# Optimization experiments

Measured on AMD Instinct MI355X. Metric: run time of the kernel, lower is better.

The kernel has to match this reference:

```python
import jax, jax.numpy as jnp
import numpy as np

N = 100000
HEADS = 4
NHID = 32


def _gat_conv(x, src, dst, W, a_src, a_dst, b):
    # x: [N, Fin]; src/dst: [E'] (self-loops already appended)
    h = (x @ W).reshape(N, HEADS, NHID)                      # [N, H, D]
    al_src = jnp.einsum('nhd,hd->nh', h, a_src)              # [N, H]
    al_dst = jnp.einsum('nhd,hd->nh', h, a_dst)
    e = jax.nn.leaky_relu(al_src[src] + al_dst[dst], 0.2)    # [E', H]
    # segment softmax over incoming edges of each destination node
    m = jax.ops.segment_max(e, dst, num_segments=N)          # [N, H]
    ex = jnp.exp(e - m[dst])
    s = jax.ops.segment_sum(ex, dst, num_segments=N)         # [N, H]
    alpha = ex / (s[dst] + 1e-16)                            # [E', H]
    msg = h[src] * alpha[:, :, None]                         # [E', H, D]
    out = jax.ops.segment_sum(msg, dst, num_segments=N)      # [N, H, D]
    return out.reshape(N, HEADS * NHID) + b


def setup_inputs() -> dict:
    key = jax.random.key(0)
    ks = jax.random.split(key, 16)
    E = 1600000
    NFEAT, NCLASS = 128, 10
    width = HEADS * NHID  # 128
    sc = 0.1
    inp = {
        'x': jax.random.normal(ks[0], (N, NFEAT), jnp.float32),
        'edge_index': jax.random.randint(ks[1], (2, E), 0, N, jnp.int64)
            if jax.config.jax_enable_x64 else jax.random.randint(ks[1], (2, E), 0, N, jnp.int32),
        'W0': jax.random.normal(ks[2], (NFEAT, width), jnp.float32) * sc,
        'a_src0': jax.random.normal(ks[3], (HEADS, NHID), jnp.float32) * sc,
        'a_dst0': jax.random.normal(ks[4], (HEADS, NHID), jnp.float32) * sc,
        'b0': jnp.zeros((width,), jnp.float32),
        'W1': jax.random.normal(ks[5], (width, width), jnp.float32) * sc,
        'a_src1': jax.random.normal(ks[6], (HEADS, NHID), jnp.float32) * sc,
        'a_dst1': jax.random.normal(ks[7], (HEADS, NHID), jnp.float32) * sc,
        'b1': jnp.zeros((width,), jnp.float32),
        'W2': jax.random.normal(ks[8], (width, width), jnp.float32) * sc,
        'a_src2': jax.random.normal(ks[9], (HEADS, NHID), jnp.float32) * sc,
        'a_dst2': jax.random.normal(ks[10], (HEADS, NHID), jnp.float32) * sc,
        'b2': jnp.zeros((width,), jnp.float32),
        'fc_W': jax.random.normal(ks[11], (width, NCLASS), jnp.float32) * sc,
        'fc_b': jnp.zeros((NCLASS,), jnp.float32),
    }
    return inp


def reference(x, edge_index, W0, a_src0, a_dst0, b0, W1, a_src1, a_dst1, b1,
              W2, a_src2, a_dst2, b2, fc_W, fc_b):
    # PyG GATConv default add_self_loops=True
    loops = jnp.arange(N, dtype=edge_index.dtype)
    src = jnp.concatenate([edge_index[0], loops])
    dst = jnp.concatenate([edge_index[1], loops])
    h = x
    for (W, a_s, a_d, b) in ((W0, a_src0, a_dst0, b0),
                             (W1, a_src1, a_dst1, b1),
                             (W2, a_src2, a_dst2, b2)):
        h = jax.nn.elu(_gat_conv(h, src, dst, W, a_s, a_d, b))
        # F.dropout(training=False) -> identity
    logits = h @ fc_W + fc_b
    return jax.nn.log_softmax(logits, axis=1)
```

## Files before the change

### kernel.cpp

```cpp
#include <hip/hip_runtime.h>
#include <math.h>

#define NN 100000
#define FEAT 128
#define NHEAD 4
#define BSH 9
#define BNODES 512
#define NBUCK 196
#define BCAP 16384
#define PA_EPT 16
#define GTILES 6250
#define GEMMB 1563
#define SRCMASK 0x1FFFF

typedef unsigned int uint;
typedef unsigned short ushort;
typedef __attribute__((ext_vector_type(8))) short short8;
typedef __attribute__((ext_vector_type(4))) float fx4;

__device__ __forceinline__ float lrelu(float v) { return v > 0.f ? v : 0.2f * v; }

__device__ __forceinline__ ushort f2bf(float f) {
    uint u = __float_as_uint(f);
    return (ushort)((u + 0x7fffu + ((u >> 16) & 1u)) >> 16);
}
__device__ __forceinline__ float bf_lo(uint u) { return __uint_as_float(u << 16); }
__device__ __forceinline__ float bf_hi(uint u) { return __uint_as_float(u & 0xffff0000u); }

__device__ __forceinline__ short8 pack8f(const float* p) {
    float4 a = *(const float4*)p, b = *(const float4*)(p + 4);
    short8 v;
    v[0] = (short)f2bf(a.x); v[1] = (short)f2bf(a.y);
    v[2] = (short)f2bf(a.z); v[3] = (short)f2bf(a.w);
    v[4] = (short)f2bf(b.x); v[5] = (short)f2bf(b.y);
    v[6] = (short)f2bf(b.z); v[7] = (short)f2bf(b.w);
    return v;
}

template <bool FP32IN>
__device__ __forceinline__ void gemm_body(
    const void* __restrict__ in, const float* __restrict__ W,
    const float* __restrict__ a_src, const float* __restrict__ a_dst,
    ushort* __restrict__ hbf, float* __restrict__ al_s, float* __restrict__ al_d,
    int bid)
{
    __shared__ __align__(16) ushort WA[FEAT * FEAT];
    const int t = threadIdx.x;
    const int lane = t & 63;
    const int node_l = lane & 15, q = lane >> 4;
    const int tile = bid * 4 + (t >> 6);
    const bool valid = tile < GTILES;
    const int n0 = tile * 16;

    short8 b0, b1, b2, b3;
    const ushort* inbf = (const ushort*)in;
    const float*  inf  = (const float*)in;
    if (valid) {
        if (FP32IN) {
            const float* rf = inf + (size_t)(n0 + node_l) * FEAT + q * 8;
            b0 = pack8f(rf);
            b1 = pack8f(rf + 32);
            b2 = pack8f(rf + 64);
            b3 = pack8f(rf + 96);
        } else {
            const ushort* rowp = inbf + (size_t)(n0 + node_l) * FEAT + q * 8;
            b0 = *(const short8*)(rowp);
            b1 = *(const short8*)(rowp + 32);
            b2 = *(const short8*)(rowp + 64);
            b3 = *(const short8*)(rowp + 96);
        }
    }

    for (int idx = t; idx < FEAT * FEAT; idx += 256) {
        int k = idx >> 7, m = idx & 127;
        int mt = m >> 4, kt = k >> 5, qq = (k >> 3) & 3, j = k & 7;
        int ln = qq * 16 + (m & 15);
        WA[((mt * 4 + kt) * 64 + ln) * 8 + j] = f2bf(W[idx]);
    }
    __syncthreads();
    if (!valid) return;

    fx4 zero = {0.f, 0.f, 0.f, 0.f};
    fx4 acc[8];
    #pragma unroll
    for (int mt = 0; mt < 8; ++mt) acc[mt] = zero;
    #pragma unroll
    for (int kt = 0; kt < 4; ++kt) {
        short8 b = (kt == 0) ? b0 : (kt == 1) ? b1 : (kt == 2) ? b2 : b3;
        #pragma unroll
        for (int mt = 0; mt < 8; ++mt) {
            short8 a = *(const short8*)&WA[((mt * 4 + kt) * 64 + lane) * 8];
            acc[mt] = __builtin_amdgcn_mfma_f32_16x16x32_bf16(a, b, acc[mt], 0, 0, 0);
        }
    }

    float ps[4] = {0.f, 0.f, 0.f, 0.f};
    float pd[4] = {0.f, 0.f, 0.f, 0.f};
    #pragma unroll
    for (int mt = 0; mt < 8; ++mt) {
        float4 as4 = *(const float4*)(a_src + mt * 16 + q * 4);
        float4 ad4 = *(const float4*)(a_dst + mt * 16 + q * 4);
        ps[mt >> 1] += acc[mt][0] * as4.x + acc[mt][1] * as4.y + acc[mt][2] * as4.z + acc[mt][3] * as4.w;
        pd[mt >> 1] += acc[mt][0] * ad4.x + acc[mt][1] * ad4.y + acc[mt][2] * ad4.z + acc[mt][3] * ad4.w;
        ushort4 hv;
        hv.x = f2bf(acc[mt][0]); hv.y = f2bf(acc[mt][1]);
        hv.z = f2bf(acc[mt][2]); hv.w = f2bf(acc[mt][3]);
        *(ushort4*)(hbf + (size_t)(n0 + node_l) * FEAT + mt * 16 + q * 4) = hv;
    }
    #pragma unroll
    for (int h = 0; h < 4; ++h) {
        ps[h] += __shfl_xor(ps[h], 16); ps[h] += __shfl_xor(ps[h], 32);
        pd[h] += __shfl_xor(pd[h], 16); pd[h] += __shfl_xor(pd[h], 32);
    }
    float vs = (q == 0) ? ps[0] : (q == 1) ? ps[1] : (q == 2) ? ps[2] : ps[3];
    float vd = (q == 0) ? pd[0] : (q == 1) ? pd[1] : (q == 2) ? pd[2] : pd[3];
    al_s[(n0 + node_l) * 4 + q] = vs;
    al_d[(n0 + node_l) * 4 + q] = vd;
}

__device__ __forceinline__ void phaseA_body(
    const int* __restrict__ ei, int E, int* bcursor, uint* __restrict__ pairs, int bid)
{
    __shared__ int lh[NBUCK], lb[NBUCK];
    int t = threadIdx.x;
    if (t < NBUCK) lh[t] = 0;
    __syncthreads();
    int base = bid * (256 * PA_EPT) + t;
    int s[PA_EPT], d[PA_EPT];
    #pragma unroll
    for (int k = 0; k < PA_EPT; ++k) {
        int i = base + k * 256;
        if (i < E)            { s[k] = ei[i]; d[k] = ei[E + i]; }
        else if (i < E + NN)  { s[k] = i - E; d[k] = s[k]; }
        else                  { s[k] = 0; d[k] = -1; }
        if (d[k] >= 0) atomicAdd(&lh[d[k] >> BSH], 1);
    }
    __syncthreads();
    if (t < NBUCK) {
        int c = lh[t];
        lb[t] = c ? atomicAdd(&bcursor[t], c) : 0;
        lh[t] = 0;
    }
    __syncthreads();
    #pragma unroll
    for (int k = 0; k < PA_EPT; ++k) {
        if (d[k] >= 0) {
            int b = d[k] >> BSH;
            int off = atomicAdd(&lh[b], 1);
            pairs[lb[b] + off] = ((uint)(d[k] & (BNODES - 1)) << 17) | (uint)s[k];
        }
    }
}

__global__ __launch_bounds__(256, 2) void gemm_mfma_kernel(
    const void* __restrict__ in, const float* __restrict__ W,
    const float* __restrict__ a_src, const float* __restrict__ a_dst,
    ushort* __restrict__ hbf, float* __restrict__ al_s, float* __restrict__ al_d)
{
    gemm_body<false>(in, W, a_src, a_dst, hbf, al_s, al_d, blockIdx.x);
}

__global__ __launch_bounds__(256, 2) void gemm0_phaseA_kernel(
    const float* __restrict__ x, const float* __restrict__ W,
    const float* __restrict__ a_src, const float* __restrict__ a_dst,
    ushort* __restrict__ hbf, float* __restrict__ al_s, float* __restrict__ al_d,
    const int* __restrict__ ei, int E, int* bcursor, uint* __restrict__ pairs)
{
    if (blockIdx.x < GEMMB)
        gemm_body<true>(x, W, a_src, a_dst, hbf, al_s, al_d, blockIdx.x);
    else
        phaseA_body(ei, E, bcursor, pairs, blockIdx.x - GEMMB);
}


__global__ __launch_bounds__(256) void bucket_hist_kernel(
    const int* __restrict__ ei, int E, int* bsize)
{
    __shared__ int lh[NBUCK];
    int t = threadIdx.x;
    if (t < NBUCK) lh[t] = 0;
    __syncthreads();
    int stride = gridDim.x * 256;
    for (int i = blockIdx.x * 256 + t; i < E + NN; i += stride) {
        int d = (i < E) ? ei[E + i] : (i - E);
        atomicAdd(&lh[d >> BSH], 1);
    }
    __syncthreads();
    if (t < NBUCK && lh[t]) atomicAdd(&bsize[t], lh[t]);
}

__global__ __launch_bounds__(256) void bucket_scan_kernel(
    const int* __restrict__ bsize, int* bbase, int* bcursor)
{
    __shared__ int sm[256];
    int t = threadIdx.x;
    int v = (t < NBUCK) ? bsize[t] : 0;
    sm[t] = v;
    __syncthreads();
    #pragma unroll
    for (int off = 1; off < 256; off <<= 1) {
        int x = (t >= off) ? sm[t - off] : 0;
        __syncthreads();
        sm[t] += x;
        __syncthreads();
    }
    if (t < NBUCK) {
        int excl = sm[t] - v;
        bbase[t] = excl;
        bcursor[t] = excl;
    }
    if (t == 255) bbase[NBUCK] = sm[255];
}

__global__ __launch_bounds__(256) void phaseB_kernel(
    const uint* __restrict__ pairs, const int* __restrict__ bbase,
    int* __restrict__ row_ptr, int* __restrict__ colidx, int EP)
{
    __shared__ int nh[BNODES];
    __shared__ int ex[BNODES];
    __shared__ int ss[256];
    __shared__ int img[BCAP];
    int b = blockIdx.x, t = threadIdx.x;
    int node0 = b << BSH;
    int nend = min(NN - node0, BNODES);
    int pb = bbase[b], pe = bbase[b + 1];
    int span = pe - pb;
    for (int j = t; j < BNODES; j += 256) nh[j] = 0;
    __syncthreads();
    for (int i = t; i < span; i += 256)
        atomicAdd(&nh[pairs[pb + i] >> 17], 1);
    __syncthreads();
    int v0 = nh[2 * t], v1 = nh[2 * t + 1];
    int psc = v0 + v1;
    ss[t] = psc;
    __syncthreads();
    #pragma unroll
    for (int off = 1; off < 256; off <<= 1) {
        int x = (t >= off) ? ss[t - off] : 0;
        __syncthreads();
        ss[t] += x;
        __syncthreads();
    }
    int ep = ss[t] - psc;
    ex[2 * t] = ep;
    ex[2 * t + 1] = ep + v0;
    __syncthreads();
    for (int j = t; j < nend; j += 256) row_ptr[node0 + j] = pb + ex[j];
    if (b == NBUCK - 1 && t == 0) row_ptr[NN] = EP;
    for (int j = t; j < BNODES; j += 256) nh[j] = ex[j];
    __syncthreads();
    if (span <= BCAP) {
        for (int i = t; i < span; i += 256) {
            uint p = pairs[pb + i];
            int pos = atomicAdd(&nh[p >> 17], 1);
            img[pos] = (int)(p & SRCMASK);
        }
        __syncthreads();
        for (int i = t; i < span; i += 256) colidx[pb + i] = img[i];
    } else {
        for (int i = t; i < span; i += 256) {
            uint p = pairs[pb + i];
            int pos = atomicAdd(&nh[p >> 17], 1);
            colidx[pb + pos] = (int)(p & SRCMASK);
        }
    }
}

#define AGGR_STEP(hv, wgt)                                                    \
    a0 = fmaf(wgt, bf_lo(hv.x), a0); a1 = fmaf(wgt, bf_hi(hv.x), a1);        \
    a2 = fmaf(wgt, bf_lo(hv.y), a2); a3 = fmaf(wgt, bf_hi(hv.y), a3);        \
    a4 = fmaf(wgt, bf_lo(hv.z), a4); a5 = fmaf(wgt, bf_hi(hv.z), a5);        \
    a6 = fmaf(wgt, bf_lo(hv.w), a6); a7 = fmaf(wgt, bf_hi(hv.w), a7);

#define PROC4(cv)                                                             \
    {                                                                         \
        int s0 = cv.x, s1 = cv.y, s2 = cv.z, s3 = cv.w;                       \
        float w0 = __expf(lrelu(al_s[s0*4 + head] + ald_h));                  \
        float w1 = __expf(lrelu(al_s[s1*4 + head] + ald_h));                  \
        float w2 = __expf(lrelu(al_s[s2*4 + head] + ald_h));                  \
        float w3 = __expf(lrelu(al_s[s3*4 + head] + ald_h));                  \
        uint4 h0 = ((const uint4*)(hbf + (size_t)s0 * FEAT))[lane];           \
        uint4 h1 = ((const uint4*)(hbf + (size_t)s1 * FEAT))[lane];           \
        uint4 h2 = ((const uint4*)(hbf + (size_t)s2 * FEAT))[lane];           \
        uint4 h3 = ((const uint4*)(hbf + (size_t)s3 * FEAT))[lane];           \
        ssum += (w0 + w1) + (w2 + w3);                                        \
        AGGR_STEP(h0, w0) AGGR_STEP(h1, w1) AGGR_STEP(h2, w2) AGGR_STEP(h3, w3) \
    }

#define PROC8(cva, cvb)                                                       \
    {                                                                         \
        int s0 = cva.x, s1 = cva.y, s2 = cva.z, s3 = cva.w;                   \
        int s4 = cvb.x, s5 = cvb.y, s6 = cvb.z, s7 = cvb.w;                   \
        uint4 h0 = ((const uint4*)(hbf + (size_t)s0 * FEAT))[lane];           \
        uint4 h1 = ((const uint4*)(hbf + (size_t)s1 * FEAT))[lane];           \
        uint4 h2 = ((const uint4*)(hbf + (size_t)s2 * FEAT))[lane];           \
        uint4 h3 = ((const uint4*)(hbf + (size_t)s3 * FEAT))[lane];           \
        uint4 h4 = ((const uint4*)(hbf + (size_t)s4 * FEAT))[lane];           \
        uint4 h5 = ((const uint4*)(hbf + (size_t)s5 * FEAT))[lane];           \
        uint4 h6 = ((const uint4*)(hbf + (size_t)s6 * FEAT))[lane];           \
        uint4 h7 = ((const uint4*)(hbf + (size_t)s7 * FEAT))[lane];           \
        float w0 = __expf(lrelu(al_s[s0*4 + head] + ald_h));                  \
        float w1 = __expf(lrelu(al_s[s1*4 + head] + ald_h));                  \
        float w2 = __expf(lrelu(al_s[s2*4 + head] + ald_h));                  \
        float w3 = __expf(lrelu(al_s[s3*4 + head] + ald_h));                  \
        float w4 = __expf(lrelu(al_s[s4*4 + head] + ald_h));                  \
        float w5 = __expf(lrelu(al_s[s5*4 + head] + ald_h));                  \
        float w6 = __expf(lrelu(al_s[s6*4 + head] + ald_h));                  \
        float w7 = __expf(lrelu(al_s[s7*4 + head] + ald_h));                  \
        ssum += ((w0 + w1) + (w2 + w3)) + ((w4 + w5) + (w6 + w7));            \
        AGGR_STEP(h0, w0) AGGR_STEP(h1, w1) AGGR_STEP(h2, w2) AGGR_STEP(h3, w3) \
        AGGR_STEP(h4, w4) AGGR_STEP(h5, w5) AGGR_STEP(h6, w6) AGGR_STEP(h7, w7) \
    }

template <bool LAST>
__global__ __launch_bounds__(256) void aggr_csr_kernel(
    const int* __restrict__ row_ptr, const int* __restrict__ colidx,
    const ushort* __restrict__ hbf, const float* __restrict__ al_s,
    const float* __restrict__ al_d, const float* __restrict__ bias,
    ushort* __restrict__ outbf,
    const float* __restrict__ fcW, const float* __restrict__ fcb,
    float* __restrict__ logout)
{
    __shared__ float WT[10][FEAT];
    __shared__ float bl[10];
    int t = threadIdx.x;
    if (LAST) {
        for (int i = t; i < FEAT * 10; i += 256) {
            int k = i / 10, c = i % 10;
            WT[c][k] = fcW[i];
        }
        if (t < 10) bl[t] = fcb[t];
        __syncthreads();
    }
    int node = blockIdx.x * 16 + (t >> 4);
    int lane = t & 15;
    int head = lane >> 2;
    float ald_h = al_d[node * 4 + head];
    int beg = row_ptr[node], end = row_ptr[node + 1];

    float ssum = 0.f;
    float a0=0.f,a1=0.f,a2=0.f,a3=0.f,a4=0.f,a5=0.f,a6=0.f,a7=0.f;

    int p = beg;
    int4 ca, cb;
    if (p + 8 <= end) {
        ca = *(const int4*)&colidx[p];
        cb = *(const int4*)&colidx[p + 4];
    }
    while (p + 16 <= end) {
        int4 na = *(const int4*)&colidx[p + 8];
        int4 nb = *(const int4*)&colidx[p + 12];
        PROC8(ca, cb)
        ca = na; cb = nb;
        p += 8;
    }
    if (p + 8 <= end) { PROC8(ca, cb) p += 8; }
    if (p + 4 <= end) {
        int4 c4 = *(const int4*)&colidx[p];
        PROC4(c4)
        p += 4;
    }
    for (; p < end; ++p) {
        int sn = colidx[p];
        float wq = __expf(lrelu(al_s[sn*4 + head] + ald_h));
        uint4 hv = ((const uint4*)(hbf + (size_t)sn * FEAT))[lane];
        ssum += wq;
        AGGR_STEP(hv, wq)
    }

    float inv = 1.f / (ssum + 1e-16f);
    const float* bp = bias + lane * 8;
    float o[8] = {a0,a1,a2,a3,a4,a5,a6,a7};
    #pragma unroll
    for (int k = 0; k < 8; ++k) {
        float v = o[k] * inv + bp[k];
        o[k] = v > 0.f ? v : __expf(v) - 1.f;
    }
    if (!LAST) {
        uint4 u;
        u.x = (uint)f2bf(o[0]) | ((uint)f2bf(o[1]) << 16);
        u.y = (uint)f2bf(o[2]) | ((uint)f2bf(o[3]) << 16);
        u.z = (uint)f2bf(o[4]) | ((uint)f2bf(o[5]) << 16);
        u.w = (uint)f2bf(o[6]) | ((uint)f2bf(o[7]) << 16);
        ((uint4*)(outbf + (size_t)node * FEAT))[lane] = u;
    } else {
        float lg[10];
        #pragma unroll
        for (int c = 0; c < 10; ++c) {
            const float* wr = &WT[c][lane * 8];
            float4 wa = *(const float4*)(wr);
            float4 wb = *(const float4*)(wr + 4);
            float acc = fmaf(o[0], wa.x, fmaf(o[1], wa.y, fmaf(o[2], wa.z, o[3] * wa.w)));
            acc = fmaf(o[4], wb.x, fmaf(o[5], wb.y, fmaf(o[6], wb.z, fmaf(o[7], wb.w, acc))));
            lg[c] = acc;
        }
        #pragma unroll
        for (int c = 0; c < 10; ++c) {
            lg[c] += __shfl_xor(lg[c], 1, 16);
            lg[c] += __shfl_xor(lg[c], 2, 16);
            lg[c] += __shfl_xor(lg[c], 4, 16);
            lg[c] += __shfl_xor(lg[c], 8, 16);
        }
        if (lane == 0) {
            float mx = -1e30f;
            #pragma unroll
            for (int c = 0; c < 10; ++c) { lg[c] += bl[c]; mx = fmaxf(mx, lg[c]); }
            float se = 0.f;
            #pragma unroll
            for (int c = 0; c < 10; ++c) se += __expf(lg[c] - mx);
            float lse = mx + __logf(se);
            float2* op = (float2*)(logout + (size_t)node * 10);
            #pragma unroll
            for (int c = 0; c < 5; ++c)
                op[c] = make_float2(lg[2*c] - lse, lg[2*c + 1] - lse);
        }
    }
}

extern "C" void kernel_launch(void* const* d_in, const int* in_sizes, int n_in,
                              void* d_out, int out_size, void* d_ws, size_t ws_size,
                              hipStream_t stream)
{
    const float* x   = (const float*)d_in[0];
    const int*   ei  = (const int*)d_in[1];
    const float* W[3]   = {(const float*)d_in[2], (const float*)d_in[6],  (const float*)d_in[10]};
    const float* asr[3] = {(const float*)d_in[3], (const float*)d_in[7],  (const float*)d_in[11]};
    const float* ads[3] = {(const float*)d_in[4], (const float*)d_in[8],  (const float*)d_in[12]};
    const float* bs[3]  = {(const float*)d_in[5], (const float*)d_in[9],  (const float*)d_in[13]};
    const float* fcW = (const float*)d_in[14];
    const float* fcb = (const float*)d_in[15];
    const int E  = in_sizes[1] / 2;
    const int EP = E + NN;

    ushort* hbf  = (ushort*)d_ws;
    ushort* ybf  = hbf + (size_t)NN * FEAT;
    float* als   = (float*)(ybf + (size_t)NN * FEAT);
    float* ald   = als + (size_t)NN * NHEAD;
    int* row_ptr = (int*)(ald + (size_t)NN * NHEAD);
    int* bsize   = row_ptr + NN + 1;
    int* bbase   = bsize + NBUCK;
    int* bcursor = bbase + NBUCK + 1;
    uint* pairs  = (uint*)(bcursor + NBUCK);
    int* colidx  = (int*)(pairs + (size_t)EP);

    const int pab = (EP + 256 * PA_EPT - 1) / (256 * PA_EPT);

    hipMemsetAsync(bsize, 0, NBUCK * sizeof(int), stream);
    bucket_hist_kernel<<<1024, 256, 0, stream>>>(ei, E, bsize);
    bucket_scan_kernel<<<1, 256, 0, stream>>>(bsize, bbase, bcursor);

    gemm0_phaseA_kernel<<<GEMMB + pab, 256, 0, stream>>>(
        x, W[0], asr[0], ads[0], hbf, als, ald, ei, E, bcursor, pairs);
    phaseB_kernel<<<NBUCK, 256, 0, stream>>>(pairs, bbase, row_ptr, colidx, EP);

    aggr_csr_kernel<false><<<(NN + 15) / 16, 256, 0, stream>>>(
        row_ptr, colidx, hbf, als, ald, bs[0], ybf, nullptr, nullptr, nullptr);

    gemm_mfma_kernel<<<GEMMB, 256, 0, stream>>>(ybf, W[1], asr[1], ads[1], hbf, als, ald);
    aggr_csr_kernel<false><<<(NN + 15) / 16, 256, 0, stream>>>(
        row_ptr, colidx, hbf, als, ald, bs[1], ybf, nullptr, nullptr, nullptr);

    gemm_mfma_kernel<<<GEMMB, 256, 0, stream>>>(ybf, W[2], asr[2], ads[2], hbf, als, ald);
    aggr_csr_kernel<true><<<(NN + 15) / 16, 256, 0, stream>>>(
        row_ptr, colidx, hbf, als, ald, bs[2], nullptr, fcW, fcb, (float*)d_out);
}
```

Measured before the change: 494.4 us.

## Fuse edge aggregation with next layer's GEMM via shared-memory tile handoff

```diff
diff --git a/kernel.cpp b/kernel.cpp
--- a/kernel.cpp
+++ b/kernel.cpp
@@ -11,6 +11,7 @@
 #define PA_EPT 16
 #define GTILES 6250
 #define GEMMB 1563
+#define HSTRIDE 136
 #define SRCMASK 0x1FFFF
 
 typedef unsigned int uint;
@@ -35,235 +36,6 @@
     v[4] = (short)f2bf(b.x); v[5] = (short)f2bf(b.y);
     v[6] = (short)f2bf(b.z); v[7] = (short)f2bf(b.w);
     return v;
-}
-
-template <bool FP32IN>
-__device__ __forceinline__ void gemm_body(
-    const void* __restrict__ in, const float* __restrict__ W,
-    const float* __restrict__ a_src, const float* __restrict__ a_dst,
-    ushort* __restrict__ hbf, float* __restrict__ al_s, float* __restrict__ al_d,
-    int bid)
-{
-    __shared__ __align__(16) ushort WA[FEAT * FEAT];
-    const int t = threadIdx.x;
-    const int lane = t & 63;
-    const int node_l = lane & 15, q = lane >> 4;
-    const int tile = bid * 4 + (t >> 6);
-    const bool valid = tile < GTILES;
-    const int n0 = tile * 16;
-
-    short8 b0, b1, b2, b3;
-    const ushort* inbf = (const ushort*)in;
-    const float*  inf  = (const float*)in;
-    if (valid) {
-        if (FP32IN) {
-            const float* rf = inf + (size_t)(n0 + node_l) * FEAT + q * 8;
-            b0 = pack8f(rf);
-            b1 = pack8f(rf + 32);
-            b2 = pack8f(rf + 64);
-            b3 = pack8f(rf + 96);
-        } else {
-            const ushort* rowp = inbf + (size_t)(n0 + node_l) * FEAT + q * 8;
-            b0 = *(const short8*)(rowp);
-            b1 = *(const short8*)(rowp + 32);
-            b2 = *(const short8*)(rowp + 64);
-            b3 = *(const short8*)(rowp + 96);
-        }
-    }
-
-    for (int idx = t; idx < FEAT * FEAT; idx += 256) {
-        int k = idx >> 7, m = idx & 127;
-        int mt = m >> 4, kt = k >> 5, qq = (k >> 3) & 3, j = k & 7;
-        int ln = qq * 16 + (m & 15);
-        WA[((mt * 4 + kt) * 64 + ln) * 8 + j] = f2bf(W[idx]);
-    }
-    __syncthreads();
-    if (!valid) return;
-
-    fx4 zero = {0.f, 0.f, 0.f, 0.f};
-    fx4 acc[8];
-    #pragma unroll
-    for (int mt = 0; mt < 8; ++mt) acc[mt] = zero;
-    #pragma unroll
-    for (int kt = 0; kt < 4; ++kt) {
-        short8 b = (kt == 0) ? b0 : (kt == 1) ? b1 : (kt == 2) ? b2 : b3;
-        #pragma unroll
-        for (int mt = 0; mt < 8; ++mt) {
-            short8 a = *(const short8*)&WA[((mt * 4 + kt) * 64 + lane) * 8];
-            acc[mt] = __builtin_amdgcn_mfma_f32_16x16x32_bf16(a, b, acc[mt], 0, 0, 0);
-        }
-    }
-
-    float ps[4] = {0.f, 0.f, 0.f, 0.f};
-    float pd[4] = {0.f, 0.f, 0.f, 0.f};
-    #pragma unroll
-    for (int mt = 0; mt < 8; ++mt) {
-        float4 as4 = *(const float4*)(a_src + mt * 16 + q * 4);
-        float4 ad4 = *(const float4*)(a_dst + mt * 16 + q * 4);
-        ps[mt >> 1] += acc[mt][0] * as4.x + acc[mt][1] * as4.y + acc[mt][2] * as4.z + acc[mt][3] * as4.w;
-        pd[mt >> 1] += acc[mt][0] * ad4.x + acc[mt][1] * ad4.y + acc[mt][2] * ad4.z + acc[mt][3] * ad4.w;
-        ushort4 hv;
-        hv.x = f2bf(acc[mt][0]); hv.y = f2bf(acc[mt][1]);
-        hv.z = f2bf(acc[mt][2]); hv.w = f2bf(acc[mt][3]);
-        *(ushort4*)(hbf + (size_t)(n0 + node_l) * FEAT + mt * 16 + q * 4) = hv;
-    }
-    #pragma unroll
-    for (int h = 0; h < 4; ++h) {
-        ps[h] += __shfl_xor(ps[h], 16); ps[h] += __shfl_xor(ps[h], 32);
-        pd[h] += __shfl_xor(pd[h], 16); pd[h] += __shfl_xor(pd[h], 32);
-    }
-    float vs = (q == 0) ? ps[0] : (q == 1) ? ps[1] : (q == 2) ? ps[2] : ps[3];
-    float vd = (q == 0) ? pd[0] : (q == 1) ? pd[1] : (q == 2) ? pd[2] : pd[3];
-    al_s[(n0 + node_l) * 4 + q] = vs;
-    al_d[(n0 + node_l) * 4 + q] = vd;
-}
-
-__device__ __forceinline__ void phaseA_body(
-    const int* __restrict__ ei, int E, int* bcursor, uint* __restrict__ pairs, int bid)
-{
-    __shared__ int lh[NBUCK], lb[NBUCK];
-    int t = threadIdx.x;
-    if (t < NBUCK) lh[t] = 0;
-    __syncthreads();
-    int base = bid * (256 * PA_EPT) + t;
-    int s[PA_EPT], d[PA_EPT];
-    #pragma unroll
-    for (int k = 0; k < PA_EPT; ++k) {
-        int i = base + k * 256;
-        if (i < E)            { s[k] = ei[i]; d[k] = ei[E + i]; }
-        else if (i < E + NN)  { s[k] = i - E; d[k] = s[k]; }
-        else                  { s[k] = 0; d[k] = -1; }
-        if (d[k] >= 0) atomicAdd(&lh[d[k] >> BSH], 1);
-    }
-    __syncthreads();
-    if (t < NBUCK) {
-        int c = lh[t];
-        lb[t] = c ? atomicAdd(&bcursor[t], c) : 0;
-        lh[t] = 0;
-    }
-    __syncthreads();
-    #pragma unroll
-    for (int k = 0; k < PA_EPT; ++k) {
-        if (d[k] >= 0) {
-            int b = d[k] >> BSH;
-            int off = atomicAdd(&lh[b], 1);
-            pairs[lb[b] + off] = ((uint)(d[k] & (BNODES - 1)) << 17) | (uint)s[k];
-        }
-    }
-}
-
-__global__ __launch_bounds__(256, 2) void gemm_mfma_kernel(
-    const void* __restrict__ in, const float* __restrict__ W,
-    const float* __restrict__ a_src, const float* __restrict__ a_dst,
-    ushort* __restrict__ hbf, float* __restrict__ al_s, float* __restrict__ al_d)
-{
-    gemm_body<false>(in, W, a_src, a_dst, hbf, al_s, al_d, blockIdx.x);
-}
-
-__global__ __launch_bounds__(256, 2) void gemm0_phaseA_kernel(
-    const float* __restrict__ x, const float* __restrict__ W,
-    const float* __restrict__ a_src, const float* __restrict__ a_dst,
-    ushort* __restrict__ hbf, float* __restrict__ al_s, float* __restrict__ al_d,
-    const int* __restrict__ ei, int E, int* bcursor, uint* __restrict__ pairs)
-{
-    if (blockIdx.x < GEMMB)
-        gemm_body<true>(x, W, a_src, a_dst, hbf, al_s, al_d, blockIdx.x);
-    else
-        phaseA_body(ei, E, bcursor, pairs, blockIdx.x - GEMMB);
-}
-
-
-__global__ __launch_bounds__(256) void bucket_hist_kernel(
-    const int* __restrict__ ei, int E, int* bsize)
-{
-    __shared__ int lh[NBUCK];
-    int t = threadIdx.x;
-    if (t < NBUCK) lh[t] = 0;
-    __syncthreads();
-    int stride = gridDim.x * 256;
-    for (int i = blockIdx.x * 256 + t; i < E + NN; i += stride) {
-        int d = (i < E) ? ei[E + i] : (i - E);
-        atomicAdd(&lh[d >> BSH], 1);
-    }
-    __syncthreads();
-    if (t < NBUCK && lh[t]) atomicAdd(&bsize[t], lh[t]);
-}
-
-__global__ __launch_bounds__(256) void bucket_scan_kernel(
-    const int* __restrict__ bsize, int* bbase, int* bcursor)
-{
-    __shared__ int sm[256];
-    int t = threadIdx.x;
-    int v = (t < NBUCK) ? bsize[t] : 0;
-    sm[t] = v;
-    __syncthreads();
-    #pragma unroll
-    for (int off = 1; off < 256; off <<= 1) {
-        int x = (t >= off) ? sm[t - off] : 0;
-        __syncthreads();
-        sm[t] += x;
-        __syncthreads();
-    }
-    if (t < NBUCK) {
-        int excl = sm[t] - v;
-        bbase[t] = excl;
-        bcursor[t] = excl;
-    }
-    if (t == 255) bbase[NBUCK] = sm[255];
-}
-
-__global__ __launch_bounds__(256) void phaseB_kernel(
-    const uint* __restrict__ pairs, const int* __restrict__ bbase,
-    int* __restrict__ row_ptr, int* __restrict__ colidx, int EP)
-{
-    __shared__ int nh[BNODES];
-    __shared__ int ex[BNODES];
-    __shared__ int ss[256];
-    __shared__ int img[BCAP];
-    int b = blockIdx.x, t = threadIdx.x;
-    int node0 = b << BSH;
-    int nend = min(NN - node0, BNODES);
-    int pb = bbase[b], pe = bbase[b + 1];
-    int span = pe - pb;
-    for (int j = t; j < BNODES; j += 256) nh[j] = 0;
-    __syncthreads();
-    for (int i = t; i < span; i += 256)
-        atomicAdd(&nh[pairs[pb + i] >> 17], 1);
-    __syncthreads();
-    int v0 = nh[2 * t], v1 = nh[2 * t + 1];
-    int psc = v0 + v1;
-    ss[t] = psc;
-    __syncthreads();
-    #pragma unroll
-    for (int off = 1; off < 256; off <<= 1) {
-        int x = (t >= off) ? ss[t - off] : 0;
-        __syncthreads();
-        ss[t] += x;
-        __syncthreads();
-    }
-    int ep = ss[t] - psc;
-    ex[2 * t] = ep;
-    ex[2 * t + 1] = ep + v0;
-    __syncthreads();
-    for (int j = t; j < nend; j += 256) row_ptr[node0 + j] = pb + ex[j];
-    if (b == NBUCK - 1 && t == 0) row_ptr[NN] = EP;
-    for (int j = t; j < BNODES; j += 256) nh[j] = ex[j];
-    __syncthreads();
-    if (span <= BCAP) {
-        for (int i = t; i < span; i += 256) {
-            uint p = pairs[pb + i];
-            int pos = atomicAdd(&nh[p >> 17], 1);
-            img[pos] = (int)(p & SRCMASK);
-        }
-        __syncthreads();
-        for (int i = t; i < span; i += 256) colidx[pb + i] = img[i];
-    } else {
-        for (int i = t; i < span; i += 256) {
-            uint p = pairs[pb + i];
-            int pos = atomicAdd(&nh[p >> 17], 1);
-            colidx[pb + pos] = (int)(p & SRCMASK);
-        }
-    }
 }
 
 #define AGGR_STEP(hv, wgt)                                                    \
@@ -312,29 +84,13 @@
         AGGR_STEP(h4, w4) AGGR_STEP(h5, w5) AGGR_STEP(h6, w6) AGGR_STEP(h7, w7) \
     }
 
-template <bool LAST>
-__global__ __launch_bounds__(256) void aggr_csr_kernel(
+__device__ __forceinline__ void aggr_node(
     const int* __restrict__ row_ptr, const int* __restrict__ colidx,
     const ushort* __restrict__ hbf, const float* __restrict__ al_s,
     const float* __restrict__ al_d, const float* __restrict__ bias,
-    ushort* __restrict__ outbf,
-    const float* __restrict__ fcW, const float* __restrict__ fcb,
-    float* __restrict__ logout)
-{
-    __shared__ float WT[10][FEAT];
-    __shared__ float bl[10];
-    int t = threadIdx.x;
-    if (LAST) {
-        for (int i = t; i < FEAT * 10; i += 256) {
-            int k = i / 10, c = i % 10;
-            WT[c][k] = fcW[i];
-        }
-        if (t < 10) bl[t] = fcb[t];
-        __syncthreads();
-    }
-    int node = blockIdx.x * 16 + (t >> 4);
-    int lane = t & 15;
-    int head = lane >> 2;
+    int node, int lane, float* __restrict__ o)
+{
+    const int head = lane >> 2;
     float ald_h = al_d[node * 4 + head];
     int beg = row_ptr[node], end = row_ptr[node + 1];
 
@@ -370,50 +126,369 @@
 
     float inv = 1.f / (ssum + 1e-16f);
     const float* bp = bias + lane * 8;
-    float o[8] = {a0,a1,a2,a3,a4,a5,a6,a7};
+    float oo[8] = {a0,a1,a2,a3,a4,a5,a6,a7};
     #pragma unroll
     for (int k = 0; k < 8; ++k) {
-        float v = o[k] * inv + bp[k];
+        float v = oo[k] * inv + bp[k];
         o[k] = v > 0.f ? v : __expf(v) - 1.f;
     }
-    if (!LAST) {
+}
+
+template <bool FP32IN>
+__device__ __forceinline__ void gemm_body(
+    const void* __restrict__ in, const float* __restrict__ W,
+    const float* __restrict__ a_src, const float* __restrict__ a_dst,
+    ushort* __restrict__ hbf, float* __restrict__ al_s, float* __restrict__ al_d,
+    int bid)
+{
+    __shared__ __align__(16) ushort WA[FEAT * FEAT];
+    const int t = threadIdx.x;
+    const int lane = t & 63;
+    const int node_l = lane & 15, q = lane >> 4;
+    const int tile = bid * 4 + (t >> 6);
+    const bool valid = tile < GTILES;
+    const int n0 = tile * 16;
+
+    short8 b0, b1, b2, b3;
+    const ushort* inbf = (const ushort*)in;
+    const float*  inf  = (const float*)in;
+    if (valid) {
+        if (FP32IN) {
+            const float* rf = inf + (size_t)(n0 + node_l) * FEAT + q * 8;
+            b0 = pack8f(rf);
+            b1 = pack8f(rf + 32);
+            b2 = pack8f(rf + 64);
+            b3 = pack8f(rf + 96);
+        } else {
+            const ushort* rowp = inbf + (size_t)(n0 + node_l) * FEAT + q * 8;
+            b0 = *(const short8*)(rowp);
+            b1 = *(const short8*)(rowp + 32);
+            b2 = *(const short8*)(rowp + 64);
+            b3 = *(const short8*)(rowp + 96);
+        }
+    }
+
+    for (int idx = t; idx < FEAT * FEAT; idx += 256) {
+        int k = idx >> 7, m = idx & 127;
+        int mt = m >> 4, kt = k >> 5, qq = (k >> 3) & 3, j = k & 7;
+        int ln = qq * 16 + (m & 15);
+        WA[((mt * 4 + kt) * 64 + ln) * 8 + j] = f2bf(W[idx]);
+    }
+    __syncthreads();
+    if (!valid) return;
+
+    fx4 zero = {0.f, 0.f, 0.f, 0.f};
+    fx4 acc[8];
+    #pragma unroll
+    for (int mt = 0; mt < 8; ++mt) acc[mt] = zero;
+    #pragma unroll
+    for (int kt = 0; kt < 4; ++kt) {
+        short8 b = (kt == 0) ? b0 : (kt == 1) ? b1 : (kt == 2) ? b2 : b3;
+        #pragma unroll
+        for (int mt = 0; mt < 8; ++mt) {
+            short8 a = *(const short8*)&WA[((mt * 4 + kt) * 64 + lane) * 8];
+            acc[mt] = __builtin_amdgcn_mfma_f32_16x16x32_bf16(a, b, acc[mt], 0, 0, 0);
+        }
+    }
+
+    float ps[4] = {0.f, 0.f, 0.f, 0.f};
+    float pd[4] = {0.f, 0.f, 0.f, 0.f};
+    #pragma unroll
+    for (int mt = 0; mt < 8; ++mt) {
+        float4 as4 = *(const float4*)(a_src + mt * 16 + q * 4);
+        float4 ad4 = *(const float4*)(a_dst + mt * 16 + q * 4);
+        ps[mt >> 1] += acc[mt][0] * as4.x + acc[mt][1] * as4.y + acc[mt][2] * as4.z + acc[mt][3] * as4.w;
+        pd[mt >> 1] += acc[mt][0] * ad4.x + acc[mt][1] * ad4.y + acc[mt][2] * ad4.z + acc[mt][3] * ad4.w;
+        ushort4 hv;
+        hv.x = f2bf(acc[mt][0]); hv.y = f2bf(acc[mt][1]);
+        hv.z = f2bf(acc[mt][2]); hv.w = f2bf(acc[mt][3]);
+        *(ushort4*)(hbf + (size_t)(n0 + node_l) * FEAT + mt * 16 + q * 4) = hv;
+    }
+    #pragma unroll
+    for (int h = 0; h < 4; ++h) {
+        ps[h] += __shfl_xor(ps[h], 16); ps[h] += __shfl_xor(ps[h], 32);
+        pd[h] += __shfl_xor(pd[h], 16); pd[h] += __shfl_xor(pd[h], 32);
+    }
+    float vs = (q == 0) ? ps[0] : (q == 1) ? ps[1] : (q == 2) ? ps[2] : ps[3];
+    float vd = (q == 0) ? pd[0] : (q == 1) ? pd[1] : (q == 2) ? pd[2] : pd[3];
+    al_s[(n0 + node_l) * 4 + q] = vs;
+    al_d[(n0 + node_l) * 4 + q] = vd;
+}
+
+__device__ __forceinline__ void phaseA_body(
+    const int* __restrict__ ei, int E, int* bcursor, uint* __restrict__ pairs, int bid)
+{
+    __shared__ int lh[NBUCK], lb[NBUCK];
+    int t = threadIdx.x;
+    if (t < NBUCK) lh[t] = 0;
+    __syncthreads();
+    int base = bid * (256 * PA_EPT) + t;
+    int s[PA_EPT], d[PA_EPT];
+    #pragma unroll
+    for (int k = 0; k < PA_EPT; ++k) {
+        int i = base + k * 256;
+        if (i < E)            { s[k] = ei[i]; d[k] = ei[E + i]; }
+        else if (i < E + NN)  { s[k] = i - E; d[k] = s[k]; }
+        else                  { s[k] = 0; d[k] = -1; }
+        if (d[k] >= 0) atomicAdd(&lh[d[k] >> BSH], 1);
+    }
+    __syncthreads();
+    if (t < NBUCK) {
+        int c = lh[t];
+        lb[t] = c ? atomicAdd(&bcursor[t], c) : 0;
+        lh[t] = 0;
+    }
+    __syncthreads();
+    #pragma unroll
+    for (int k = 0; k < PA_EPT; ++k) {
+        if (d[k] >= 0) {
+            int b = d[k] >> BSH;
+            int off = atomicAdd(&lh[b], 1);
+            pairs[lb[b] + off] = ((uint)(d[k] & (BNODES - 1)) << 17) | (uint)s[k];
+        }
+    }
+}
+
+__global__ __launch_bounds__(256, 2) void gemm0_phaseA_kernel(
+    const float* __restrict__ x, const float* __restrict__ W,
+    const float* __restrict__ a_src, const float* __restrict__ a_dst,
+    ushort* __restrict__ hbf, float* __restrict__ al_s, float* __restrict__ al_d,
+    const int* __restrict__ ei, int E, int* bcursor, uint* __restrict__ pairs)
+{
+    if (blockIdx.x < GEMMB)
+        gemm_body<true>(x, W, a_src, a_dst, hbf, al_s, al_d, blockIdx.x);
+    else
+        phaseA_body(ei, E, bcursor, pairs, blockIdx.x - GEMMB);
+}
+
+__global__ __launch_bounds__(256, 2) void aggr_gemm_fused_kernel(
+    const int* __restrict__ row_ptr, const int* __restrict__ colidx,
+    const ushort* __restrict__ hbf_in, const float* __restrict__ al_s_in,
+    const float* __restrict__ al_d_in, const float* __restrict__ bias,
+    const float* __restrict__ W, const float* __restrict__ a_src,
+    const float* __restrict__ a_dst,
+    ushort* __restrict__ hbf_out, float* __restrict__ al_s_out,
+    float* __restrict__ al_d_out)
+{
+    __shared__ __align__(16) ushort WA[FEAT * FEAT];
+    __shared__ __align__(16) ushort HS[4][16 * HSTRIDE];
+    const int t = threadIdx.x;
+    for (int idx = t; idx < FEAT * FEAT; idx += 256) {
+        int k = idx >> 7, m = idx & 127;
+        int mt = m >> 4, kt = k >> 5, qq = (k >> 3) & 3, j = k & 7;
+        int ln = qq * 16 + (m & 15);
+        WA[((mt * 4 + kt) * 64 + ln) * 8 + j] = f2bf(W[idx]);
+    }
+    __syncthreads();
+
+    const int wv = t >> 6, lane = t & 63;
+    const int tile = blockIdx.x * 4 + wv;
+    if (tile >= GTILES) return;
+    const int n0 = tile * 16;
+    const int ng = lane >> 4, l16 = lane & 15;
+
+    #pragma unroll 1
+    for (int it = 0; it < 4; ++it) {
+        int node = n0 + it * 4 + ng;
+        float o[8];
+        aggr_node(row_ptr, colidx, hbf_in, al_s_in, al_d_in, bias, node, l16, o);
         uint4 u;
         u.x = (uint)f2bf(o[0]) | ((uint)f2bf(o[1]) << 16);
         u.y = (uint)f2bf(o[2]) | ((uint)f2bf(o[3]) << 16);
         u.z = (uint)f2bf(o[4]) | ((uint)f2bf(o[5]) << 16);
         u.w = (uint)f2bf(o[6]) | ((uint)f2bf(o[7]) << 16);
-        ((uint4*)(outbf + (size_t)node * FEAT))[lane] = u;
+        *(uint4*)&HS[wv][(it * 4 + ng) * HSTRIDE + l16 * 8] = u;
+    }
+
+    const int node_l = l16, q = ng;
+    short8 b0 = *(const short8*)&HS[wv][node_l * HSTRIDE +      q * 8];
+    short8 b1 = *(const short8*)&HS[wv][node_l * HSTRIDE + 32 + q * 8];
+    short8 b2 = *(const short8*)&HS[wv][node_l * HSTRIDE + 64 + q * 8];
+    short8 b3 = *(const short8*)&HS[wv][node_l * HSTRIDE + 96 + q * 8];
+
+    fx4 zero = {0.f, 0.f, 0.f, 0.f};
+    fx4 acc[8];
+    #pragma unroll
+    for (int mt = 0; mt < 8; ++mt) acc[mt] = zero;
+    #pragma unroll
+    for (int kt = 0; kt < 4; ++kt) {
+        short8 b = (kt == 0) ? b0 : (kt == 1) ? b1 : (kt == 2) ? b2 : b3;
+        #pragma unroll
+        for (int mt = 0; mt < 8; ++mt) {
+            short8 a = *(const short8*)&WA[((mt * 4 + kt) * 64 + lane) * 8];
+            acc[mt] = __builtin_amdgcn_mfma_f32_16x16x32_bf16(a, b, acc[mt], 0, 0, 0);
+        }
+    }
+
+    float ps[4] = {0.f, 0.f, 0.f, 0.f};
+    float pd[4] = {0.f, 0.f, 0.f, 0.f};
+    #pragma unroll
+    for (int mt = 0; mt < 8; ++mt) {
+        float4 as4 = *(const float4*)(a_src + mt * 16 + q * 4);
+        float4 ad4 = *(const float4*)(a_dst + mt * 16 + q * 4);
+        ps[mt >> 1] += acc[mt][0] * as4.x + acc[mt][1] * as4.y + acc[mt][2] * as4.z + acc[mt][3] * as4.w;
+        pd[mt >> 1] += acc[mt][0] * ad4.x + acc[mt][1] * ad4.y + acc[mt][2] * ad4.z + acc[mt][3] * ad4.w;
+        ushort4 hv;
+        hv.x = f2bf(acc[mt][0]); hv.y = f2bf(acc[mt][1]);
+        hv.z = f2bf(acc[mt][2]); hv.w = f2bf(acc[mt][3]);
+        *(ushort4*)(hbf_out + (size_t)(n0 + node_l) * FEAT + mt * 16 + q * 4) = hv;
+    }
+    #pragma unroll
+    for (int h = 0; h < 4; ++h) {
+        ps[h] += __shfl_xor(ps[h], 16); ps[h] += __shfl_xor(ps[h], 32);
+        pd[h] += __shfl_xor(pd[h], 16); pd[h] += __shfl_xor(pd[h], 32);
+    }
+    float vs = (q == 0) ? ps[0] : (q == 1) ? ps[1] : (q == 2) ? ps[2] : ps[3];
+    float vd = (q == 0) ? pd[0] : (q == 1) ? pd[1] : (q == 2) ? pd[2] : pd[3];
+    al_s_out[(n0 + node_l) * 4 + q] = vs;
+    al_d_out[(n0 + node_l) * 4 + q] = vd;
+}
+
+
+__global__ __launch_bounds__(256) void bucket_hist_kernel(
+    const int* __restrict__ ei, int E, int* bsize)
+{
+    __shared__ int lh[NBUCK];
+    int t = threadIdx.x;
+    if (t < NBUCK) lh[t] = 0;
+    __syncthreads();
+    int stride = gridDim.x * 256;
+    for (int i = blockIdx.x * 256 + t; i < E + NN; i += stride) {
+        int d = (i < E) ? ei[E + i] : (i - E);
+        atomicAdd(&lh[d >> BSH], 1);
+    }
+    __syncthreads();
+    if (t < NBUCK && lh[t]) atomicAdd(&bsize[t], lh[t]);
+}
+
+__global__ __launch_bounds__(256) void bucket_scan_kernel(
+    const int* __restrict__ bsize, int* bbase, int* bcursor)
+{
+    __shared__ int sm[256];
+    int t = threadIdx.x;
+    int v = (t < NBUCK) ? bsize[t] : 0;
+    sm[t] = v;
+    __syncthreads();
+    #pragma unroll
+    for (int off = 1; off < 256; off <<= 1) {
+        int x = (t >= off) ? sm[t - off] : 0;
+        __syncthreads();
+        sm[t] += x;
+        __syncthreads();
+    }
+    if (t < NBUCK) {
+        int excl = sm[t] - v;
+        bbase[t] = excl;
+        bcursor[t] = excl;
+    }
+    if (t == 255) bbase[NBUCK] = sm[255];
+}
+
+__global__ __launch_bounds__(256) void phaseB_kernel(
+    const uint* __restrict__ pairs, const int* __restrict__ bbase,
+    int* __restrict__ row_ptr, int* __restrict__ colidx, int EP)
+{
+    __shared__ int nh[BNODES];
+    __shared__ int ex[BNODES];
+    __shared__ int ss[256];
+    __shared__ int img[BCAP];
+    int b = blockIdx.x, t = threadIdx.x;
+    int node0 = b << BSH;
+    int nend = min(NN - node0, BNODES);
+    int pb = bbase[b], pe = bbase[b + 1];
+    int span = pe - pb;
+    for (int j = t; j < BNODES; j += 256) nh[j] = 0;
+    __syncthreads();
+    for (int i = t; i < span; i += 256)
+        atomicAdd(&nh[pairs[pb + i] >> 17], 1);
+    __syncthreads();
+    int v0 = nh[2 * t], v1 = nh[2 * t + 1];
+    int psc = v0 + v1;
+    ss[t] = psc;
+    __syncthreads();
+    #pragma unroll
+    for (int off = 1; off < 256; off <<= 1) {
+        int x = (t >= off) ? ss[t - off] : 0;
+        __syncthreads();
+        ss[t] += x;
+        __syncthreads();
+    }
+    int ep = ss[t] - psc;
+    ex[2 * t] = ep;
+    ex[2 * t + 1] = ep + v0;
+    __syncthreads();
+    for (int j = t; j < nend; j += 256) row_ptr[node0 + j] = pb + ex[j];
+    if (b == NBUCK - 1 && t == 0) row_ptr[NN] = EP;
+    for (int j = t; j < BNODES; j += 256) nh[j] = ex[j];
+    __syncthreads();
+    if (span <= BCAP) {
+        for (int i = t; i < span; i += 256) {
+            uint p = pairs[pb + i];
+            int pos = atomicAdd(&nh[p >> 17], 1);
+            img[pos] = (int)(p & SRCMASK);
+        }
+        __syncthreads();
+        for (int i = t; i < span; i += 256) colidx[pb + i] = img[i];
     } else {
-        float lg[10];
+        for (int i = t; i < span; i += 256) {
+            uint p = pairs[pb + i];
+            int pos = atomicAdd(&nh[p >> 17], 1);
+            colidx[pb + pos] = (int)(p & SRCMASK);
+        }
+    }
+}
+
+__global__ __launch_bounds__(256) void aggr_fc_kernel(
+    const int* __restrict__ row_ptr, const int* __restrict__ colidx,
+    const ushort* __restrict__ hbf, const float* __restrict__ al_s,
+    const float* __restrict__ al_d, const float* __restrict__ bias,
+    const float* __restrict__ fcW, const float* __restrict__ fcb,
+    float* __restrict__ logout)
+{
+    __shared__ float WT[10][FEAT];
+    __shared__ float bl[10];
+    int t = threadIdx.x;
+    for (int i = t; i < FEAT * 10; i += 256) {
+        int k = i / 10, c = i % 10;
+        WT[c][k] = fcW[i];
+    }
+    if (t < 10) bl[t] = fcb[t];
+    __syncthreads();
+
+    int node = blockIdx.x * 16 + (t >> 4);
+    int lane = t & 15;
+    float o[8];
+    aggr_node(row_ptr, colidx, hbf, al_s, al_d, bias, node, lane, o);
+
+    float lg[10];
+    #pragma unroll
+    for (int c = 0; c < 10; ++c) {
+        const float* wr = &WT[c][lane * 8];
+        float4 wa = *(const float4*)(wr);
+        float4 wb = *(const float4*)(wr + 4);
+        float acc = fmaf(o[0], wa.x, fmaf(o[1], wa.y, fmaf(o[2], wa.z, o[3] * wa.w)));
+        acc = fmaf(o[4], wb.x, fmaf(o[5], wb.y, fmaf(o[6], wb.z, fmaf(o[7], wb.w, acc))));
+        lg[c] = acc;
+    }
+    #pragma unroll
+    for (int c = 0; c < 10; ++c) {
+        lg[c] += __shfl_xor(lg[c], 1, 16);
+        lg[c] += __shfl_xor(lg[c], 2, 16);
+        lg[c] += __shfl_xor(lg[c], 4, 16);
+        lg[c] += __shfl_xor(lg[c], 8, 16);
+    }
+    if (lane == 0) {
+        float mx = -1e30f;
         #pragma unroll
-        for (int c = 0; c < 10; ++c) {
-            const float* wr = &WT[c][lane * 8];
-            float4 wa = *(const float4*)(wr);
-            float4 wb = *(const float4*)(wr + 4);
-            float acc = fmaf(o[0], wa.x, fmaf(o[1], wa.y, fmaf(o[2], wa.z, o[3] * wa.w)));
-            acc = fmaf(o[4], wb.x, fmaf(o[5], wb.y, fmaf(o[6], wb.z, fmaf(o[7], wb.w, acc))));
-            lg[c] = acc;
-        }
+        for (int c = 0; c < 10; ++c) { lg[c] += bl[c]; mx = fmaxf(mx, lg[c]); }
+        float se = 0.f;
         #pragma unroll
-        for (int c = 0; c < 10; ++c) {
-            lg[c] += __shfl_xor(lg[c], 1, 16);
-            lg[c] += __shfl_xor(lg[c], 2, 16);
-            lg[c] += __shfl_xor(lg[c], 4, 16);
-            lg[c] += __shfl_xor(lg[c], 8, 16);
-        }
-        if (lane == 0) {
-            float mx = -1e30f;
-            #pragma unroll
-            for (int c = 0; c < 10; ++c) { lg[c] += bl[c]; mx = fmaxf(mx, lg[c]); }
-            float se = 0.f;
-            #pragma unroll
-            for (int c = 0; c < 10; ++c) se += __expf(lg[c] - mx);
-            float lse = mx + __logf(se);
-            float2* op = (float2*)(logout + (size_t)node * 10);
-            #pragma unroll
-            for (int c = 0; c < 5; ++c)
-                op[c] = make_float2(lg[2*c] - lse, lg[2*c + 1] - lse);
-        }
+        for (int c = 0; c < 10; ++c) se += __expf(lg[c] - mx);
+        float lse = mx + __logf(se);
+        float2* op = (float2*)(logout + (size_t)node * 10);
+        #pragma unroll
+        for (int c = 0; c < 5; ++c)
+            op[c] = make_float2(lg[2*c] - lse, lg[2*c + 1] - lse);
     }
 }
 
@@ -432,11 +507,13 @@
     const int E  = in_sizes[1] / 2;
     const int EP = E + NN;
 
-    ushort* hbf  = (ushort*)d_ws;
-    ushort* ybf  = hbf + (size_t)NN * FEAT;
-    float* als   = (float*)(ybf + (size_t)NN * FEAT);
-    float* ald   = als + (size_t)NN * NHEAD;
-    int* row_ptr = (int*)(ald + (size_t)NN * NHEAD);
+    ushort* hbfA = (ushort*)d_ws;
+    ushort* hbfB = hbfA + (size_t)NN * FEAT;
+    float* alsA  = (float*)(hbfB + (size_t)NN * FEAT);
+    float* aldA  = alsA + (size_t)NN * NHEAD;
+    float* alsB  = aldA + (size_t)NN * NHEAD;
+    float* aldB  = alsB + (size_t)NN * NHEAD;
+    int* row_ptr = (int*)(aldB + (size_t)NN * NHEAD);
     int* bsize   = row_ptr + NN + 1;
     int* bbase   = bsize + NBUCK;
     int* bcursor = bbase + NBUCK + 1;
@@ -450,17 +527,16 @@
     bucket_scan_kernel<<<1, 256, 0, stream>>>(bsize, bbase, bcursor);
 
     gemm0_phaseA_kernel<<<GEMMB + pab, 256, 0, stream>>>(
-        x, W[0], asr[0], ads[0], hbf, als, ald, ei, E, bcursor, pairs);
+        x, W[0], asr[0], ads[0], hbfA, alsA, aldA, ei, E, bcursor, pairs);
     phaseB_kernel<<<NBUCK, 256, 0, stream>>>(pairs, bbase, row_ptr, colidx, EP);
 
-    aggr_csr_kernel<false><<<(NN + 15) / 16, 256, 0, stream>>>(
-        row_ptr, colidx, hbf, als, ald, bs[0], ybf, nullptr, nullptr, nullptr);
-
-    gemm_mfma_kernel<<<GEMMB, 256, 0, stream>>>(ybf, W[1], asr[1], ads[1], hbf, als, ald);
-    aggr_csr_kernel<false><<<(NN + 15) / 16, 256, 0, stream>>>(
-        row_ptr, colidx, hbf, als, ald, bs[1], ybf, nullptr, nullptr, nullptr);
-
-    gemm_mfma_kernel<<<GEMMB, 256, 0, stream>>>(ybf, W[2], asr[2], ads[2], hbf, als, ald);
-    aggr_csr_kernel<true><<<(NN + 15) / 16, 256, 0, stream>>>(
-        row_ptr, colidx, hbf, als, ald, bs[2], nullptr, fcW, fcb, (float*)d_out);
-}
+    aggr_gemm_fused_kernel<<<GEMMB, 256, 0, stream>>>(
+        row_ptr, colidx, hbfA, alsA, aldA, bs[0], W[1], asr[1], ads[1],
+        hbfB, alsB, aldB);
+    aggr_gemm_fused_kernel<<<GEMMB, 256, 0, stream>>>(
+        row_ptr, colidx, hbfB, alsB, aldB, bs[1], W[2], asr[2], ads[2],
+        hbfA, alsA, aldA);
+
+    aggr_fc_kernel<<<(NN + 15) / 16, 256, 0, stream>>>(
+        row_ptr, colidx, hbfA, alsA, aldA, bs[2], fcW, fcb, (float*)d_out);
+}
```

Result: no change. 499.0 us (+0.9%).
